# Optimization experiments

Hardware: AMD Instinct MI355X
Metric: run time of the kernel (lower is better)

The kernel has to match this reference:

```python
import jax, jax.numpy as jnp
import numpy as np

D_MODEL = 512
NUM_HEADS = 8
D_HEAD = 64
B, T = 8, 1024


def sinusoidal_pos(start, end, d, dtype=jnp.float32):
    # positions start .. end-1, standard sinusoidal encoding, shape (1, end-start, d)
    pos = jnp.arange(start, end, dtype=jnp.float32)[:, None]              # (L,1)
    inv_freq = jnp.exp(-jnp.log(10000.0) * jnp.arange(0, d, 2, dtype=jnp.float32) / d)
    ang = pos * inv_freq[None, :]                                          # (L,d/2)
    pe = jnp.stack([jnp.sin(ang), jnp.cos(ang)], axis=-1).reshape(pos.shape[0], d)
    return pe[None].astype(dtype)                                          # (1,L,d)


def _relative_shift(x):
    # x: (B,H,T,L) -> Transformer-XL shift trick
    b, h, t, l = x.shape
    x = jnp.pad(x, ((0, 0), (0, 0), (0, 0), (1, 0)))                       # (B,H,T,L+1)
    x = x.reshape(b, h, l + 1, t)[:, :, 1:, :].reshape(b, h, t, l)
    return x


def setup_inputs() -> dict:
    key = jax.random.key(0)
    ks = jax.random.split(key, 8)
    hd = NUM_HEADS * D_HEAD
    s_in = 1.0 / np.sqrt(D_MODEL)
    s_out = 1.0 / np.sqrt(hd)
    return {
        "xs": jax.random.normal(ks[0], (B, T, D_MODEL), jnp.float32),
        "mask": jnp.ones((B, T, T), jnp.int32),
        "Wq": jax.random.normal(ks[1], (D_MODEL, hd), jnp.float32) * s_in,
        "Wk": jax.random.normal(ks[2], (D_MODEL, hd), jnp.float32) * s_in,
        "Wv": jax.random.normal(ks[3], (D_MODEL, hd), jnp.float32) * s_in,
        "Wpos": jax.random.normal(ks[4], (D_MODEL, hd), jnp.float32) * s_in,
        "Wout": jax.random.normal(ks[5], (hd, D_MODEL), jnp.float32) * s_out,
        "u_bias": jax.random.normal(ks[6], (NUM_HEADS, D_HEAD), jnp.float32) * 0.02,
        "v_bias": jax.random.normal(ks[7], (NUM_HEADS, D_HEAD), jnp.float32) * 0.02,
    }


def reference(xs, mask, Wq, Wk, Wv, Wpos, Wout, u_bias, v_bias):
    b, t, _ = xs.shape
    scale = 1.0 / np.sqrt(D_HEAD)

    def split_heads(y):  # (B,T,H*dh) -> (B,H,T,dh)
        return y.reshape(b, t, NUM_HEADS, D_HEAD).transpose(0, 2, 1, 3)

    q = split_heads(xs @ Wq)
    k = split_heads(xs @ Wk)
    v = split_heads(xs @ Wv)

    # positions -(T-1) .. T-1, length 2T-1
    pos_enc = sinusoidal_pos(-(t - 1), t, D_MODEL, xs.dtype)               # (1,L,D)
    p = (pos_enc[0] @ Wpos).reshape(-1, NUM_HEADS, D_HEAD).transpose(1, 0, 2)  # (H,L,dh)

    q_u = q + u_bias[None, :, None, :]
    q_v = q + v_bias[None, :, None, :]

    matrix_ac = jnp.einsum("bhtd,bhsd->bhts", q_u, k)                      # (B,H,T,T)
    matrix_bd = jnp.einsum("bhtd,hld->bhtl", q_v, p)                       # (B,H,T,2T-1)
    matrix_bd = _relative_shift(matrix_bd)[:, :, :, :t]                    # (B,H,T,T)

    scores = (matrix_ac + matrix_bd) * scale

    m = (mask[:, None, :, :] == 0)                                          # (B,1,T,T)
    scores = jnp.where(m, -jnp.inf, scores)
    attn = jax.nn.softmax(scores, axis=-1)
    attn = jnp.where(m, 0.0, attn)
    # dropout is identity in eval mode

    z = jnp.einsum("bhts,bhsd->bthd", attn, v).reshape(b, t, NUM_HEADS * D_HEAD)
    return z @ Wout
```

## Files before the change

kernel.cpp:

```cpp
#include <hip/hip_runtime.h>
#include <hip/hip_bf16.h>


typedef unsigned short u16;
typedef unsigned long long u64;
typedef __attribute__((ext_vector_type(8))) short bf16x8;
typedef __attribute__((ext_vector_type(8))) unsigned short ushort8v;
typedef __attribute__((ext_vector_type(4))) float floatx4;

__device__ __forceinline__ float b2f(u16 u) {
    union { unsigned int i; float f; } x; x.i = ((unsigned int)u) << 16; return x.f;
}
__device__ __forceinline__ u16 f2b(float f) {
    __hip_bfloat16 h = __float2bfloat16(f);
    return *reinterpret_cast<u16*>(&h);
}

#define MFMA16(a, b, c) __builtin_amdgcn_mfma_f32_16x16x32_bf16(a, b, c, 0, 0, 0)

__global__ __launch_bounds__(256) void prep_kernel(
    const float* __restrict__ X, u16* __restrict__ Xb,
    const float* __restrict__ W0, const float* __restrict__ W1,
    const float* __restrict__ W2, const float* __restrict__ W3,
    const float* __restrict__ W4, u16* __restrict__ WT,
    const int* __restrict__ mask, u64* __restrict__ Mp,
    u16* __restrict__ Peb)
{
    const int bi = blockIdx.x;
    const int tid = threadIdx.x;
    if (bi < 2048) {
        size_t i = ((size_t)bi * 256 + tid) * 8;
        float4 a = *(const float4*)&X[i];
        float4 b = *(const float4*)&X[i + 4];
        ushort8v s;
        s[0] = f2b(a.x); s[1] = f2b(a.y); s[2] = f2b(a.z); s[3] = f2b(a.w);
        s[4] = f2b(b.x); s[5] = f2b(b.y); s[6] = f2b(b.z); s[7] = f2b(b.w);
        *(ushort8v*)&Xb[i] = s;
    } else if (bi < 2368) {
        __shared__ float t[64][68];
        const int li = bi - 2048;
        const int m = li >> 6;
        const float* src = (m == 0) ? W0 : (m == 1) ? W1 : (m == 2) ? W2
                         : (m == 3) ? W3 : W4;
        u16* dst = WT + (size_t)m * 262144;
        const int sub = li & 63;
        const int k0 = ((sub >> 3) & 7) * 64, n0 = (sub & 7) * 64;
        const int r = tid >> 4, c = tid & 15;
#pragma unroll
        for (int rr = 0; rr < 64; rr += 16) {
            float4 v = *(const float4*)&src[(size_t)(k0 + r + rr) * 512 + n0 + 4 * c];
            t[r + rr][4 * c + 0] = v.x;
            t[r + rr][4 * c + 1] = v.y;
            t[r + rr][4 * c + 2] = v.z;
            t[r + rr][4 * c + 3] = v.w;
        }
        __syncthreads();
        const int nrow = tid >> 2, kc = (tid & 3) * 16;
        ushort8v s0, s1;
#pragma unroll
        for (int e = 0; e < 8; ++e) {
            s0[e] = f2b(t[kc + e][nrow]);
            s1[e] = f2b(t[kc + 8 + e][nrow]);
        }
        *(ushort8v*)&dst[(size_t)(n0 + nrow) * 512 + k0 + kc] = s0;
        *(ushort8v*)&dst[(size_t)(n0 + nrow) * 512 + k0 + kc + 8] = s1;
    } else if (bi < 4416) {
        const int lane = tid & 63, w = tid >> 6;
        const int row = (bi - 2368) * 4 + w;
#pragma unroll
        for (int j = 0; j < 16; ++j) {
            int v = mask[(size_t)row * 1024 + j * 64 + lane];
            u64 bits = __ballot(v != 0);
            if (lane == j) Mp[(size_t)row * 16 + j] = bits;
        }
    } else {
        const int lane = tid & 63, w = tid >> 6;
        const int l = (bi - 4416) * 4 + w;
        const int lc = (l > 2046) ? 2046 : l;
        const float pos = (float)(lc - 1023);
        ushort8v s;
#pragma unroll
        for (int e = 0; e < 8; ++e) {
            int k = (lane << 3) + e;
            int i = k >> 1;
            float invf = expf(-0.035977892f * (float)i);
            float ang = pos * invf;
            float v = (k & 1) ? cosf(ang) : sinf(ang);
            s[e] = f2b(v);
        }
        *(ushort8v*)&Peb[(size_t)l * 512 + (lane << 3)] = s;
    }
}

__global__ __launch_bounds__(256, 2) void qkv_mfma(
    const u16* __restrict__ Xb, const u16* __restrict__ WqT,
    const u16* __restrict__ WkT, const u16* __restrict__ WvT,
    const u16* __restrict__ Peb, const u16* __restrict__ WposT,
    u16* __restrict__ Qb, u16* __restrict__ Kb, u16* __restrict__ Vtg,
    u16* __restrict__ Pg)
{
    __shared__ u16 Xl[128 * 40];
    __shared__ u16 Wl[128 * 40];
    const int tid = threadIdx.x;
    const int lane = tid & 63, w = tid >> 6;
    const int quad = lane >> 4, ln = lane & 15;
    const int wm = w & 1, wn = w >> 1;

    const int yy = blockIdx.y;
    int sel, m0, n0;
    const u16 *Ap, *Bp;
    if (yy < 12) {
        sel = yy >> 2; n0 = (yy & 3) * 128; m0 = blockIdx.x * 128;
        Ap = Xb; Bp = (sel == 0) ? WqT : (sel == 1) ? WkT : WvT;
    } else {
        sel = 3; m0 = (blockIdx.x >> 2) * 128; n0 = (blockIdx.x & 3) * 128;
        Ap = Peb; Bp = WposT;
    }
    const int b = (m0 >> 10) & 7, tbase = m0 & 1023;

    const int sr = tid >> 2, sg = tid & 3;

    floatx4 acc[4][4];
#pragma unroll
    for (int i = 0; i < 4; ++i)
#pragma unroll
        for (int j = 0; j < 4; ++j) acc[i][j] = (floatx4){0.f, 0.f, 0.f, 0.f};

    ushort8v xq[2], wq2[2];
#pragma unroll
    for (int it = 0; it < 2; ++it) {
        int r = sr + it * 64;
        xq[it]  = *(const ushort8v*)&Ap[(size_t)(m0 + r) * 512 + sg * 8];
        wq2[it] = *(const ushort8v*)&Bp[(size_t)(n0 + r) * 512 + sg * 8];
    }

    for (int kc = 0; kc < 512; kc += 32) {
        __syncthreads();
#pragma unroll
        for (int it = 0; it < 2; ++it) {
            int r = sr + it * 64;
            *(ushort8v*)&Xl[r * 40 + sg * 8] = xq[it];
            *(ushort8v*)&Wl[r * 40 + sg * 8] = wq2[it];
        }
        __syncthreads();
        if (kc + 32 < 512) {
#pragma unroll
            for (int it = 0; it < 2; ++it) {
                int r = sr + it * 64;
                xq[it]  = *(const ushort8v*)&Ap[(size_t)(m0 + r) * 512 + kc + 32 + sg * 8];
                wq2[it] = *(const ushort8v*)&Bp[(size_t)(n0 + r) * 512 + kc + 32 + sg * 8];
            }
        }
        bf16x8 am[4], an[4];
#pragma unroll
        for (int i = 0; i < 4; ++i)
            am[i] = *(bf16x8*)&Xl[(wm * 64 + i * 16 + ln) * 40 + quad * 8];
#pragma unroll
        for (int j = 0; j < 4; ++j)
            an[j] = *(bf16x8*)&Wl[(wn * 64 + j * 16 + ln) * 40 + quad * 8];
        if (sel != 2) {
#pragma unroll
            for (int i = 0; i < 4; ++i)
#pragma unroll
                for (int j = 0; j < 4; ++j)
                    acc[i][j] = MFMA16(an[j], am[i], acc[i][j]);
        } else {
#pragma unroll
            for (int i = 0; i < 4; ++i)
#pragma unroll
                for (int j = 0; j < 4; ++j)
                    acc[i][j] = MFMA16(am[i], an[j], acc[i][j]);
        }
    }
    if (sel < 2) {
        u16* dst = (sel == 0) ? Qb : Kb;
#pragma unroll
        for (int i = 0; i < 4; ++i) {
            int t = tbase + wm * 64 + i * 16 + ln;
#pragma unroll
            for (int j = 0; j < 4; ++j) {
                int n = n0 + wn * 64 + j * 16 + quad * 4;
                int h = n >> 6, d = n & 63;
                ushort4 s;
                s.x = f2b(acc[i][j][0]); s.y = f2b(acc[i][j][1]);
                s.z = f2b(acc[i][j][2]); s.w = f2b(acc[i][j][3]);
                *(ushort4*)&dst[(((size_t)b * 8 + h) * 1024 + t) * 64 + d] = s;
            }
        }
    } else if (sel == 2) {
#pragma unroll
        for (int i = 0; i < 4; ++i) {
            int t4 = tbase + wm * 64 + i * 16 + quad * 4;
#pragma unroll
            for (int j = 0; j < 4; ++j) {
                int n = n0 + wn * 64 + j * 16 + ln;
                int h = n >> 6, d = n & 63;
                ushort4 s;
                s.x = f2b(acc[i][j][0]); s.y = f2b(acc[i][j][1]);
                s.z = f2b(acc[i][j][2]); s.w = f2b(acc[i][j][3]);
                *(ushort4*)&Vtg[(((size_t)b * 8 + h) * 64 + d) * 1024 + t4] = s;
            }
        }
    } else {
#pragma unroll
        for (int i = 0; i < 4; ++i) {
            int l = m0 + wm * 64 + i * 16 + ln;
#pragma unroll
            for (int j = 0; j < 4; ++j) {
                int n = n0 + wn * 64 + j * 16 + quad * 4;
                int h = n >> 6, d = n & 63;
                ushort4 s;
                s.x = f2b(acc[i][j][0]); s.y = f2b(acc[i][j][1]);
                s.z = f2b(acc[i][j][2]); s.w = f2b(acc[i][j][3]);
                *(ushort4*)&Pg[(((size_t)h << 11) + l) * 64 + d] = s;
            }
        }
    }
}

__device__ __forceinline__ bf16x8 addbias(bf16x8 q, const float* __restrict__ bias) {
    float4 a = *(const float4*)&bias[0];
    float4 b = *(const float4*)&bias[4];
    bf16x8 r;
    r[0] = (short)f2b(b2f((u16)q[0]) + a.x);
    r[1] = (short)f2b(b2f((u16)q[1]) + a.y);
    r[2] = (short)f2b(b2f((u16)q[2]) + a.z);
    r[3] = (short)f2b(b2f((u16)q[3]) + a.w);
    r[4] = (short)f2b(b2f((u16)q[4]) + b.x);
    r[5] = (short)f2b(b2f((u16)q[5]) + b.y);
    r[6] = (short)f2b(b2f((u16)q[6]) + b.z);
    r[7] = (short)f2b(b2f((u16)q[7]) + b.w);
    return r;
}

__global__ __launch_bounds__(256, 2) void attn_mfma(
    const u16* __restrict__ Qb,
    const u16* __restrict__ Kb, const u16* __restrict__ Vtg,
    const u16* __restrict__ P, const u64* __restrict__ Mp,
    const float* __restrict__ ub, const float* __restrict__ vb,
    u16* __restrict__ Z)
{
    __shared__ u16 Klds[64 * 72];
    __shared__ u16 Vtlds[64 * 72];
    __shared__ u16 Pb[192 * 64];
    __shared__ __align__(16) char WaveBuf[4][16 * 84 * 4];

    const int tid  = threadIdx.x;
    const int lane = tid & 63;
    const int w    = tid >> 6;
    const int quad = lane >> 4;
    const int ln   = lane & 15;

    const int bid = blockIdx.x;
    const int xg  = bid & 7;
    const int idx = bid >> 3;
    const int bh_i = xg * 8 + (idx >> 3);
    const int t0 = (idx & 7) << 7;
    const int h  = bh_i & 7;
    const int b  = bh_i >> 3;
    const size_t bh  = (size_t)bh_i * 1024;
    const size_t bhd = (size_t)bh_i * 64;
    size_t mprow[2];
    mprow[0] = ((size_t)b * 1024 + t0 + 16 * w + ln) * 16;
    mprow[1] = ((size_t)b * 1024 + t0 + 64 + 16 * w + ln) * 16;

    bf16x8 qu0[2], qu1[2], qv0[2], qv1[2];
#pragma unroll
    for (int c = 0; c < 2; ++c) {
        const size_t qoff = (bh + t0 + 64 * c + 16 * w + ln) * 64;
        bf16x8 q0 = *(const bf16x8*)&Qb[qoff + quad * 8];
        bf16x8 q1 = *(const bf16x8*)&Qb[qoff + 32 + quad * 8];
        qu0[c] = addbias(q0, &ub[h * 64 + quad * 8]);
        qu1[c] = addbias(q1, &ub[h * 64 + 32 + quad * 8]);
        qv0[c] = addbias(q0, &vb[h * 64 + quad * 8]);
        qv1[c] = addbias(q1, &vb[h * 64 + 32 + quad * 8]);
    }

    floatx4 O[2][4];
#pragma unroll
    for (int c = 0; c < 2; ++c)
#pragma unroll
        for (int dt = 0; dt < 4; ++dt) O[c][dt] = (floatx4){0.f, 0.f, 0.f, 0.f};
    float m_run[2] = {-3.0e38f, -3.0e38f}, l_run[2] = {0.f, 0.f};

    float* gw = (float*)&WaveBuf[w][0];
    u16*  pw  = (u16*)&WaveBuf[w][0];

    const int str = tid >> 3, stg = tid & 7;
    ushort8v kq[2], vq[2], pq[6];

#define LOAD_CHUNK(S0)                                                            \
    {                                                                             \
        _Pragma("unroll")                                                         \
        for (int it = 0; it < 2; ++it) {                                          \
            int r = str + it * 32;                                                \
            kq[it] = *(const ushort8v*)&Kb[(bh + (S0) + r) * 64 + stg * 8];       \
            vq[it] = *(const ushort8v*)&Vtg[(bhd + r) * 1024 + (S0) + stg * 8];   \
        }                                                                         \
        const int lb0 = 896 - t0 + (S0);                                          \
        _Pragma("unroll")                                                         \
        for (int it = 0; it < 6; ++it) {                                          \
            int r = str + it * 32;                                                \
            size_t l = (size_t)(lb0 + r);                                         \
            pq[it] = *(const ushort8v*)&P[((((size_t)h << 11) + l) << 6) + stg * 8]; \
        }                                                                         \
    }

    LOAD_CHUNK(0)

    for (int s0 = 0; s0 < 1024; s0 += 64) {
        __syncthreads();
#pragma unroll
        for (int it = 0; it < 2; ++it) {
            int r = str + it * 32;
            *(ushort8v*)&Klds[r * 72 + stg * 8] = kq[it];
            *(ushort8v*)&Vtlds[r * 72 + stg * 8] = vq[it];
        }
#pragma unroll
        for (int it = 0; it < 6; ++it) {
            int r = str + it * 32;
            *(ushort8v*)&Pb[r * 64 + ((stg ^ (r & 7)) << 3)] = pq[it];
        }
        __syncthreads();
        if (s0 + 64 < 1024) LOAD_CHUNK(s0 + 64)

        bf16x8 vf0[4], vf1[4];
#pragma unroll
        for (int dt = 0; dt < 4; ++dt) {
            int vr = dt * 16 + ln;
            vf0[dt] = *(bf16x8*)&Vtlds[vr * 72 + quad * 8];
            vf1[dt] = *(bf16x8*)&Vtlds[vr * 72 + 32 + quad * 8];
        }

#pragma unroll
        for (int c = 0; c < 2; ++c) {
            const u64 bits = Mp[mprow[c] + (s0 >> 6)];
            const int rb0 = 112 - 64 * c - 16 * w;
#pragma unroll
            for (int jt = 0; jt < 5; ++jt) {
                int rb = rb0 + jt * 16 + ln;
                bf16x8 a0 = *(bf16x8*)&Pb[rb * 64 + ((quad ^ (rb & 7)) << 3)];
                bf16x8 a1 = *(bf16x8*)&Pb[rb * 64 + (((4 + quad) ^ (rb & 7)) << 3)];
                floatx4 g = {0.f, 0.f, 0.f, 0.f};
                g = MFMA16(a0, qv0[c], g);
                g = MFMA16(a1, qv1[c], g);
                *(floatx4*)&gw[ln * 84 + jt * 16 + quad * 4] = g;
            }
            floatx4 cac[4];
#pragma unroll
            for (int st = 0; st < 4; ++st) {
                int kr = st * 16 + ln;
                bf16x8 a0 = *(bf16x8*)&Klds[kr * 72 + quad * 8];
                bf16x8 a1 = *(bf16x8*)&Klds[kr * 72 + 32 + quad * 8];
                floatx4 cc = {0.f, 0.f, 0.f, 0.f};
                cc = MFMA16(a0, qu0[c], cc);
                cc = MFMA16(a1, qu1[c], cc);
                cac[st] = cc;
            }
            float sc[4][4];
            float cmax = -3.0e38f;
#pragma unroll
            for (int st = 0; st < 4; ++st) {
                int j0 = st * 16 + quad * 4 + 15 - ln;
#pragma unroll
                for (int r = 0; r < 4; ++r) {
                    float v = (cac[st][r] + gw[ln * 84 + j0 + r]) * 0.125f;
                    int ss = st * 16 + quad * 4 + r;
                    v = ((bits >> ss) & 1ull) ? v : -1.0e30f;
                    sc[st][r] = v;
                    cmax = fmaxf(cmax, v);
                }
            }
            cmax = fmaxf(cmax, __shfl_xor(cmax, 16));
            cmax = fmaxf(cmax, __shfl_xor(cmax, 32));
            float m_new = fmaxf(m_run[c], cmax);
            float alpha = __expf(m_run[c] - m_new);
            float psum = 0.f;
#pragma unroll
            for (int st = 0; st < 4; ++st) {
                float p0 = __expf(sc[st][0] - m_new);
                float p1 = __expf(sc[st][1] - m_new);
                float p2 = __expf(sc[st][2] - m_new);
                float p3 = __expf(sc[st][3] - m_new);
                psum += (p0 + p1) + (p2 + p3);
                ushort4 pk;
                pk.x = f2b(p0); pk.y = f2b(p1); pk.z = f2b(p2); pk.w = f2b(p3);
                *(ushort4*)&pw[ln * 72 + st * 16 + quad * 4] = pk;
            }
            psum += __shfl_xor(psum, 16);
            psum += __shfl_xor(psum, 32);
            l_run[c] = l_run[c] * alpha + psum;
            m_run[c] = m_new;
            float a0s = __shfl(alpha, quad * 4 + 0);
            float a1s = __shfl(alpha, quad * 4 + 1);
            float a2s = __shfl(alpha, quad * 4 + 2);
            float a3s = __shfl(alpha, quad * 4 + 3);
#pragma unroll
            for (int dt = 0; dt < 4; ++dt) {
                O[c][dt][0] *= a0s; O[c][dt][1] *= a1s;
                O[c][dt][2] *= a2s; O[c][dt][3] *= a3s;
            }
            bf16x8 pa0 = *(bf16x8*)&pw[ln * 72 + quad * 8];
            bf16x8 pa1 = *(bf16x8*)&pw[ln * 72 + 32 + quad * 8];
#pragma unroll
            for (int dt = 0; dt < 4; ++dt) {
                O[c][dt] = MFMA16(pa0, vf0[dt], O[c][dt]);
                O[c][dt] = MFMA16(pa1, vf1[dt], O[c][dt]);
            }
        }
    }
#pragma unroll
    for (int c = 0; c < 2; ++c) {
        float li[4];
#pragma unroll
        for (int r = 0; r < 4; ++r) li[r] = 1.0f / __shfl(l_run[c], quad * 4 + r);
#pragma unroll
        for (int r = 0; r < 4; ++r) {
            size_t zo = ((size_t)b * 1024 + t0 + 64 * c + 16 * w + quad * 4 + r) * 512
                      + h * 64 + ln;
            Z[zo + 0]  = f2b(O[c][0][r] * li[r]);
            Z[zo + 16] = f2b(O[c][1][r] * li[r]);
            Z[zo + 32] = f2b(O[c][2][r] * li[r]);
            Z[zo + 48] = f2b(O[c][3][r] * li[r]);
        }
    }
}

__global__ __launch_bounds__(256, 2) void out_mfma(
    const u16* __restrict__ Zb, const u16* __restrict__ WoT,
    float* __restrict__ out)
{
    __shared__ u16 Xl[128 * 40];
    __shared__ u16 Wl[128 * 40];
    const int tid = threadIdx.x;
    const int lane = tid & 63, w = tid >> 6;
    const int quad = lane >> 4, ln = lane & 15;
    const int wm = w & 1, wn = w >> 1;
    const int m0 = blockIdx.x * 128;
    const int n0 = blockIdx.y * 128;
    const int sr = tid >> 2, sg = tid & 3;

    floatx4 acc[4][4];
#pragma unroll
    for (int i = 0; i < 4; ++i)
#pragma unroll
        for (int j = 0; j < 4; ++j) acc[i][j] = (floatx4){0.f, 0.f, 0.f, 0.f};

    ushort8v xq[2], wq2[2];
#pragma unroll
    for (int it = 0; it < 2; ++it) {
        int r = sr + it * 64;
        xq[it]  = *(const ushort8v*)&Zb[(size_t)(m0 + r) * 512 + sg * 8];
        wq2[it] = *(const ushort8v*)&WoT[(size_t)(n0 + r) * 512 + sg * 8];
    }

    for (int kc = 0; kc < 512; kc += 32) {
        __syncthreads();
#pragma unroll
        for (int it = 0; it < 2; ++it) {
            int r = sr + it * 64;
            *(ushort8v*)&Xl[r * 40 + sg * 8] = xq[it];
            *(ushort8v*)&Wl[r * 40 + sg * 8] = wq2[it];
        }
        __syncthreads();
        if (kc + 32 < 512) {
#pragma unroll
            for (int it = 0; it < 2; ++it) {
                int r = sr + it * 64;
                xq[it]  = *(const ushort8v*)&Zb[(size_t)(m0 + r) * 512 + kc + 32 + sg * 8];
                wq2[it] = *(const ushort8v*)&WoT[(size_t)(n0 + r) * 512 + kc + 32 + sg * 8];
            }
        }
        bf16x8 am[4], an[4];
#pragma unroll
        for (int i = 0; i < 4; ++i)
            am[i] = *(bf16x8*)&Xl[(wm * 64 + i * 16 + ln) * 40 + quad * 8];
#pragma unroll
        for (int j = 0; j < 4; ++j)
            an[j] = *(bf16x8*)&Wl[(wn * 64 + j * 16 + ln) * 40 + quad * 8];
#pragma unroll
        for (int i = 0; i < 4; ++i)
#pragma unroll
            for (int j = 0; j < 4; ++j)
                acc[i][j] = MFMA16(an[j], am[i], acc[i][j]);
    }
#pragma unroll
    for (int i = 0; i < 4; ++i) {
        int m = m0 + wm * 64 + i * 16 + ln;
#pragma unroll
        for (int j = 0; j < 4; ++j) {
            int n = n0 + wn * 64 + j * 16 + quad * 4;
            float4 s;
            s.x = acc[i][j][0]; s.y = acc[i][j][1];
            s.z = acc[i][j][2]; s.w = acc[i][j][3];
            *(float4*)&out[(size_t)m * 512 + n] = s;
        }
    }
}

extern "C" void kernel_launch(void* const* d_in, const int* in_sizes, int n_in,
                              void* d_out, int out_size, void* d_ws, size_t ws_size,
                              hipStream_t stream) {
    const float* xs   = (const float*)d_in[0];
    const int*   mask = (const int*)d_in[1];
    const float* Wq   = (const float*)d_in[2];
    const float* Wk   = (const float*)d_in[3];
    const float* Wv   = (const float*)d_in[4];
    const float* Wpos = (const float*)d_in[5];
    const float* Wout = (const float*)d_in[6];
    const float* ub   = (const float*)d_in[7];
    const float* vb   = (const float*)d_in[8];
    float* out = (float*)d_out;

    u16* Qb  = (u16*)d_ws;
    u16* Kb  = Qb + 4194304;
    u16* Vtg = Kb + 4194304;
    u16* Pg  = Vtg + 4194304;
    u16* XZ  = Pg + 1048576;
    u16* WT  = XZ + 4194304;
    u16* WqT = WT;
    u16* WkT = WT + 262144;
    u16* WvT = WT + 524288;
    u16* WoT = WT + 786432;
    u16* WposT = WT + 1048576;
    u16* Peb = WT + 1310720;
    u64* Mp  = (u64*)(Peb + 1048576);

    prep_kernel<<<4928, 256, 0, stream>>>(xs, XZ, Wq, Wk, Wv, Wout, Wpos, WT,
                                          mask, Mp, Peb);
    qkv_mfma<<<dim3(64, 13), 256, 0, stream>>>(XZ, WqT, WkT, WvT, Peb, WposT,
                                               Qb, Kb, Vtg, Pg);
    attn_mfma<<<512, 256, 0, stream>>>(Qb, Kb, Vtg, Pg, Mp, ub, vb, XZ);
    out_mfma<<<dim3(64, 4), 256, 0, stream>>>(XZ, WoT, out);
}
```

Baseline: 223.3 us.

## Stream positional rows into an LDS ring buffer via async global-to-LDS loads

The positional-projection tile becomes a 256-row circular LDS buffer. Only the 64 newly needed rows per key chunk are fetched, using global_load_lds directly into shared memory, instead of reloading all 192 rows through registers every iteration. Mask bits for the next chunk are prefetched. The 1/sqrt(d) scale is folded into the biased query vectors so the per-score multiply disappears. This cuts global traffic, VGPR staging and LDS store instructions, but relies on correct wait ordering for the async LDS writes and raises LDS use per block.

```diff
diff --git a/kernel.cpp b/kernel.cpp
--- a/kernel.cpp
+++ b/kernel.cpp
@@ -4,6 +4,7 @@
 
 typedef unsigned short u16;
 typedef unsigned long long u64;
+typedef unsigned int u32;
 typedef __attribute__((ext_vector_type(8))) short bf16x8;
 typedef __attribute__((ext_vector_type(8))) unsigned short ushort8v;
 typedef __attribute__((ext_vector_type(4))) float floatx4;
@@ -17,6 +18,12 @@
 }
 
 #define MFMA16(a, b, c) __builtin_amdgcn_mfma_f32_16x16x32_bf16(a, b, c, 0, 0, 0)
+
+__device__ __forceinline__ void gll16(const u16* g, u16* l) {
+    __builtin_amdgcn_global_load_lds(
+        (const __attribute__((address_space(1))) u32*)g,
+        (__attribute__((address_space(3))) u32*)l, 16, 0, 0);
+}
 
 __global__ __launch_bounds__(256) void prep_kernel(
     const float* __restrict__ X, u16* __restrict__ Xb,
@@ -222,14 +229,14 @@
     float4 a = *(const float4*)&bias[0];
     float4 b = *(const float4*)&bias[4];
     bf16x8 r;
-    r[0] = (short)f2b(b2f((u16)q[0]) + a.x);
-    r[1] = (short)f2b(b2f((u16)q[1]) + a.y);
-    r[2] = (short)f2b(b2f((u16)q[2]) + a.z);
-    r[3] = (short)f2b(b2f((u16)q[3]) + a.w);
-    r[4] = (short)f2b(b2f((u16)q[4]) + b.x);
-    r[5] = (short)f2b(b2f((u16)q[5]) + b.y);
-    r[6] = (short)f2b(b2f((u16)q[6]) + b.z);
-    r[7] = (short)f2b(b2f((u16)q[7]) + b.w);
+    r[0] = (short)f2b(0.125f * (b2f((u16)q[0]) + a.x));
+    r[1] = (short)f2b(0.125f * (b2f((u16)q[1]) + a.y));
+    r[2] = (short)f2b(0.125f * (b2f((u16)q[2]) + a.z));
+    r[3] = (short)f2b(0.125f * (b2f((u16)q[3]) + a.w));
+    r[4] = (short)f2b(0.125f * (b2f((u16)q[4]) + b.x));
+    r[5] = (short)f2b(0.125f * (b2f((u16)q[5]) + b.y));
+    r[6] = (short)f2b(0.125f * (b2f((u16)q[6]) + b.z));
+    r[7] = (short)f2b(0.125f * (b2f((u16)q[7]) + b.w));
     return r;
 }
 
@@ -242,7 +249,7 @@
 {
     __shared__ u16 Klds[64 * 72];
     __shared__ u16 Vtlds[64 * 72];
-    __shared__ u16 Pb[192 * 64];
+    __shared__ u16 Pb[256 * 64];
     __shared__ __align__(16) char WaveBuf[4][16 * 84 * 4];
 
     const int tid  = threadIdx.x;
@@ -260,6 +267,7 @@
     const int b  = bh_i >> 3;
     const size_t bh  = (size_t)bh_i * 1024;
     const size_t bhd = (size_t)bh_i * 64;
+    const int lbase0 = 896 - t0;
     size_t mprow[2];
     mprow[0] = ((size_t)b * 1024 + t0 + 16 * w + ln) * 16;
     mprow[1] = ((size_t)b * 1024 + t0 + 64 + 16 * w + ln) * 16;
@@ -287,26 +295,25 @@
     u16*  pw  = (u16*)&WaveBuf[w][0];
 
     const int str = tid >> 3, stg = tid & 7;
-    ushort8v kq[2], vq[2], pq[6];
-
-#define LOAD_CHUNK(S0)                                                            \
-    {                                                                             \
-        _Pragma("unroll")                                                         \
-        for (int it = 0; it < 2; ++it) {                                          \
-            int r = str + it * 32;                                                \
-            kq[it] = *(const ushort8v*)&Kb[(bh + (S0) + r) * 64 + stg * 8];       \
-            vq[it] = *(const ushort8v*)&Vtg[(bhd + r) * 1024 + (S0) + stg * 8];   \
-        }                                                                         \
-        const int lb0 = 896 - t0 + (S0);                                          \
-        _Pragma("unroll")                                                         \
-        for (int it = 0; it < 6; ++it) {                                          \
-            int r = str + it * 32;                                                \
-            size_t l = (size_t)(lb0 + r);                                         \
-            pq[it] = *(const ushort8v*)&P[((((size_t)h << 11) + l) << 6) + stg * 8]; \
-        }                                                                         \
-    }
-
-    LOAD_CHUNK(0)
+    const int g8 = lane >> 3, s8 = lane & 7;
+    const int pcol = ((s8 ^ g8) << 3);
+    ushort8v kq[2], vq[2];
+    u64 bc0, bc1;
+
+#pragma unroll
+    for (int it = 0; it < 6; ++it) {
+        int rb = lbase0 + 8 * w + 32 * it;
+        gll16(&P[(((size_t)h << 11) + (size_t)(rb + g8)) * 64 + pcol],
+              &Pb[(rb & 255) << 6]);
+    }
+#pragma unroll
+    for (int it = 0; it < 2; ++it) {
+        int r = str + it * 32;
+        kq[it] = *(const ushort8v*)&Kb[(bh + r) * 64 + stg * 8];
+        vq[it] = *(const ushort8v*)&Vtg[(bhd + r) * 1024 + stg * 8];
+    }
+    bc0 = Mp[mprow[0]];
+    bc1 = Mp[mprow[1]];
 
     for (int s0 = 0; s0 < 1024; s0 += 64) {
         __syncthreads();
@@ -316,13 +323,27 @@
             *(ushort8v*)&Klds[r * 72 + stg * 8] = kq[it];
             *(ushort8v*)&Vtlds[r * 72 + stg * 8] = vq[it];
         }
-#pragma unroll
-        for (int it = 0; it < 6; ++it) {
-            int r = str + it * 32;
-            *(ushort8v*)&Pb[r * 64 + ((stg ^ (r & 7)) << 3)] = pq[it];
-        }
-        __syncthreads();
-        if (s0 + 64 < 1024) LOAD_CHUNK(s0 + 64)
+        __syncthreads();
+
+        const int lb8 = (lbase0 + s0) & 255;
+        u64 nb0 = 0, nb1 = 0;
+        if (s0 + 64 < 1024) {
+#pragma unroll
+            for (int it = 0; it < 2; ++it) {
+                int r = str + it * 32;
+                kq[it] = *(const ushort8v*)&Kb[(bh + s0 + 64 + r) * 64 + stg * 8];
+                vq[it] = *(const ushort8v*)&Vtg[(bhd + r) * 1024 + s0 + 64 + stg * 8];
+            }
+            const int lst = lbase0 + s0 + 192;
+#pragma unroll
+            for (int it = 0; it < 2; ++it) {
+                int rb = lst + 8 * w + 32 * it;
+                gll16(&P[(((size_t)h << 11) + (size_t)(rb + g8)) * 64 + pcol],
+                      &Pb[(rb & 255) << 6]);
+            }
+            nb0 = Mp[mprow[0] + (s0 >> 6) + 1];
+            nb1 = Mp[mprow[1] + (s0 >> 6) + 1];
+        }
 
         bf16x8 vf0[4], vf1[4];
 #pragma unroll
@@ -334,13 +355,14 @@
 
 #pragma unroll
         for (int c = 0; c < 2; ++c) {
-            const u64 bits = Mp[mprow[c] + (s0 >> 6)];
+            const u64 bits = (c == 0) ? bc0 : bc1;
             const int rb0 = 112 - 64 * c - 16 * w;
 #pragma unroll
             for (int jt = 0; jt < 5; ++jt) {
                 int rb = rb0 + jt * 16 + ln;
-                bf16x8 a0 = *(bf16x8*)&Pb[rb * 64 + ((quad ^ (rb & 7)) << 3)];
-                bf16x8 a1 = *(bf16x8*)&Pb[rb * 64 + (((4 + quad) ^ (rb & 7)) << 3)];
+                int prow = ((lb8 + rb) & 255) << 6;
+                bf16x8 a0 = *(bf16x8*)&Pb[prow + ((quad ^ (rb & 7)) << 3)];
+                bf16x8 a1 = *(bf16x8*)&Pb[prow + (((4 + quad) ^ (rb & 7)) << 3)];
                 floatx4 g = {0.f, 0.f, 0.f, 0.f};
                 g = MFMA16(a0, qv0[c], g);
                 g = MFMA16(a1, qv1[c], g);
@@ -364,7 +386,7 @@
                 int j0 = st * 16 + quad * 4 + 15 - ln;
 #pragma unroll
                 for (int r = 0; r < 4; ++r) {
-                    float v = (cac[st][r] + gw[ln * 84 + j0 + r]) * 0.125f;
+                    float v = cac[st][r] + gw[ln * 84 + j0 + r];
                     int ss = st * 16 + quad * 4 + r;
                     v = ((bits >> ss) & 1ull) ? v : -1.0e30f;
                     sc[st][r] = v;
@@ -408,6 +430,7 @@
                 O[c][dt] = MFMA16(pa1, vf1[dt], O[c][dt]);
             }
         }
+        bc0 = nb0; bc1 = nb1;
     }
 #pragma unroll
     for (int c = 0; c < 2; ++c) {
```

Measured after the change: 221.1 us. No clear change (-1.0%).
